# Kernel tuning notes

Measured on AMD Instinct MI355X. Metric: run time of the kernel, lower is better.

The kernel has to match this reference:

```python
import jax, jax.numpy as jnp
import numpy as np

N = 100000
E = 1600000
H = 64      # hidden_size
NH = 8      # num_heads
DH = H // NH  # per-head dim (heads are the LAST axis, as in the torch code)


def _lin(x, W, b):
    return x @ W + b


def setup_inputs() -> dict:
    key = jax.random.key(0)
    ks = jax.random.split(key, 18)
    s = 0.05
    inp = {
        "h_x": jax.random.normal(ks[0], (N, H), jnp.float32),
        "h_e": jax.random.normal(ks[1], (E, H), jnp.float32),
        "row": jax.random.randint(ks[2], (E,), 0, N, jnp.int32),  # dst node of each nonzero
        "col": jax.random.randint(ks[3], (E,), 0, N, jnp.int32),  # src node of each nonzero
    }
    names = ["q", "k", "v", "e", "oh", "oe"]
    for i, nm in enumerate(names):
        inp["W" + nm] = jax.random.normal(ks[4 + 2 * i], (H, H), jnp.float32) * s
        inp["b" + nm] = jax.random.normal(ks[5 + 2 * i], (H,), jnp.float32) * s
    return inp


def reference(h_x, h_e, row, col, Wq, bq, Wk, bk, Wv, bv, We, be, Woh, boh, Woe, boe):
    n = h_x.shape[0]
    m = h_e.shape[0]
    q = _lin(h_x, Wq, bq).reshape(n, DH, NH)
    k = _lin(h_x, Wk, bk).reshape(n, DH, NH)
    v = _lin(h_x, Wv, bv).reshape(n, DH, NH)
    e = _lin(h_e, We, be).reshape(m, DH, NH)

    # SDDMM: per-nonzero (i=row, j=col), per-head dot of q[i] and k[j]  -> (E, NH)
    scores = (q[row] * k[col]).sum(axis=1) / jnp.sqrt(jnp.float32(DH))

    # edge gating: e.sum over dh axis -> (E, NH)
    e_gate = e.sum(axis=1)
    scores = scores * e_gate

    # oe branch (uses pre-softmax gated scores)
    oe_feat = scores[:, None, :] * e          # (E, DH, NH)
    oe = _lin(oe_feat.reshape(m, H), Woe, boe)

    # sparse softmax over dim=1 (per destination row), per head
    mx = jax.ops.segment_max(scores, row, num_segments=n)      # (N, NH)
    ex = jnp.exp(scores - mx[row])
    den = jax.ops.segment_sum(ex, row, num_segments=n)         # (N, NH)
    sm = ex / den[row]                                          # (E, NH)

    # bSpMM: h_out[i,:,h] = sum_{e: row[e]=i} sm[e,h] * v[col[e],:,h]
    h_out = jax.ops.segment_sum(sm[:, None, :] * v[col], row, num_segments=n)
    oh = _lin(h_out.reshape(n, H), Woh, boh)
    return (oh, oe)
```

## Files before the change

kernel.cpp:

```cpp
#include <hip/hip_runtime.h>

typedef __attribute__((ext_vector_type(8))) short bf16x8;
typedef __attribute__((ext_vector_type(4))) float f32x4;
typedef __attribute__((ext_vector_type(4))) unsigned short u16x4;

__device__ __forceinline__ float bf2f(unsigned short h) {
  return __uint_as_float(((unsigned)h) << 16);
}
__device__ __forceinline__ unsigned cvtpk(float a, float b) {
  unsigned r;
  asm("v_cvt_pk_bf16_f32 %0, %1, %2" : "=v"(r) : "v"(a), "v"(b));
  return r;
}
__device__ __forceinline__ unsigned short f2bf(float f) {
  return (unsigned short)(cvtpk(f, f) & 0xffffu);
}
__device__ __forceinline__ bf16x8 pack8(f32x4 x0, f32x4 x1) {
  union { bf16x8 v; unsigned u[4]; } z;
  z.u[0] = cvtpk(x0[0], x0[1]);
  z.u[1] = cvtpk(x0[2], x0[3]);
  z.u[2] = cvtpk(x1[0], x1[1]);
  z.u[3] = cvtpk(x1[2], x1[3]);
  return z.v;
}

template<bool IN_BF16, bool OUT_BF16>
__global__ void __launch_bounds__(256) gemm64_kernel(const void* __restrict__ Ain,
    const float* __restrict__ W, const float* __restrict__ bias,
    void* __restrict__ Out, int M) {
  const int tid = threadIdx.x;
  const int l = tid & 63;
  const int g = l >> 4;
  const int n15 = l & 15;

  bf16x8 bfrag[4][2];
  float bv[4];
#pragma unroll
  for (int nb = 0; nb < 4; ++nb) {
    bv[nb] = bias[nb * 16 + n15];
#pragma unroll
    for (int kb = 0; kb < 2; ++kb)
#pragma unroll
      for (int j = 0; j < 8; ++j)
        bfrag[nb][kb][j] = (short)f2bf(W[(kb * 32 + g * 8 + j) * 64 + nb * 16 + n15]);
  }

  int wid = (blockIdx.x * blockDim.x + tid) >> 6;
  int nw = (gridDim.x * blockDim.x) >> 6;
  int ntiles = (M + 15) >> 4;
  for (int t = wid; t < ntiles; t += nw) {
    int m0 = t << 4;
    int arow = m0 + n15;
    bf16x8 a0, a1;
    if (arow < M) {
      if constexpr (IN_BF16) {
        const unsigned short* ap = (const unsigned short*)Ain + (size_t)arow * 64 + g * 8;
        a0 = *(const bf16x8*)ap;
        a1 = *(const bf16x8*)(ap + 32);
      } else {
        const float* ap = (const float*)Ain + (size_t)arow * 64 + g * 8;
        a0 = pack8(*(const f32x4*)ap, *(const f32x4*)(ap + 4));
        a1 = pack8(*(const f32x4*)(ap + 32), *(const f32x4*)(ap + 36));
      }
    } else {
#pragma unroll
      for (int j = 0; j < 8; ++j) { a0[j] = 0; a1[j] = 0; }
    }
    f32x4 acc[4];
#pragma unroll
    for (int nb = 0; nb < 4; ++nb) {
      acc[nb] = (f32x4){bv[nb], bv[nb], bv[nb], bv[nb]};
      acc[nb] = __builtin_amdgcn_mfma_f32_16x16x32_bf16(a0, bfrag[nb][0], acc[nb], 0, 0, 0);
      acc[nb] = __builtin_amdgcn_mfma_f32_16x16x32_bf16(a1, bfrag[nb][1], acc[nb], 0, 0, 0);
    }
#pragma unroll
    for (int nb = 0; nb < 4; ++nb)
#pragma unroll
      for (int r = 0; r < 4; ++r) {
        int orow = m0 + g * 4 + r;
        if (orow < M) {
          float val = acc[nb][r];
          size_t oidx = (size_t)orow * 64 + nb * 16 + n15;
          if constexpr (OUT_BF16) ((unsigned short*)Out)[oidx] = f2bf(val);
          else                    ((float*)Out)[oidx] = val;
        }
      }
  }
}

__global__ void __launch_bounds__(256) qkv3_kernel(const float* __restrict__ hx,
    const float* __restrict__ Wq, const float* __restrict__ bq,
    const float* __restrict__ Wk, const float* __restrict__ bk,
    const float* __restrict__ Wv, const float* __restrict__ bv,
    unsigned short* __restrict__ q, unsigned short* __restrict__ k,
    unsigned short* __restrict__ v, int M) {
  const int tid = threadIdx.x;
  const int l = tid & 63;
  const int g = l >> 4;
  const int n15 = l & 15;
  const float* Ws[3] = {Wq, Wk, Wv};
  const float* bs[3] = {bq, bk, bv};
  unsigned short* outs[3] = {q, k, v};

  bf16x8 bfrag[3][4][2];
  float bvv[3][4];
#pragma unroll
  for (int w = 0; w < 3; ++w)
#pragma unroll
    for (int nb = 0; nb < 4; ++nb) {
      bvv[w][nb] = bs[w][nb * 16 + n15];
#pragma unroll
      for (int kb = 0; kb < 2; ++kb)
#pragma unroll
        for (int j = 0; j < 8; ++j)
          bfrag[w][nb][kb][j] = (short)f2bf(Ws[w][(kb * 32 + g * 8 + j) * 64 + nb * 16 + n15]);
    }

  int wid = (blockIdx.x * blockDim.x + tid) >> 6;
  int nw = (gridDim.x * blockDim.x) >> 6;
  int ntiles = (M + 15) >> 4;
  for (int t = wid; t < ntiles; t += nw) {
    int m0 = t << 4;
    int arow = m0 + n15;
    bf16x8 a0, a1;
    if (arow < M) {
      const float* ap = hx + (size_t)arow * 64 + g * 8;
      a0 = pack8(*(const f32x4*)ap, *(const f32x4*)(ap + 4));
      a1 = pack8(*(const f32x4*)(ap + 32), *(const f32x4*)(ap + 36));
    } else {
#pragma unroll
      for (int j = 0; j < 8; ++j) { a0[j] = 0; a1[j] = 0; }
    }
#pragma unroll
    for (int w = 0; w < 3; ++w) {
      f32x4 acc[4];
#pragma unroll
      for (int nb = 0; nb < 4; ++nb) {
        acc[nb] = (f32x4){bvv[w][nb], bvv[w][nb], bvv[w][nb], bvv[w][nb]};
        acc[nb] = __builtin_amdgcn_mfma_f32_16x16x32_bf16(a0, bfrag[w][nb][0], acc[nb], 0, 0, 0);
        acc[nb] = __builtin_amdgcn_mfma_f32_16x16x32_bf16(a1, bfrag[w][nb][1], acc[nb], 0, 0, 0);
      }
#pragma unroll
      for (int nb = 0; nb < 4; ++nb)
#pragma unroll
        for (int r = 0; r < 4; ++r) {
          int orow = m0 + g * 4 + r;
          if (orow < M)
            outs[w][(size_t)orow * 64 + nb * 16 + n15] = f2bf(acc[nb][r]);
        }
    }
  }
}

__global__ void __launch_bounds__(512) edge_fused_kernel(
    const float* __restrict__ he,
    const int* __restrict__ rowi, const int* __restrict__ coli,
    const int* __restrict__ eslot,
    const unsigned short* __restrict__ qb, const unsigned short* __restrict__ kbuf,
    const float* __restrict__ We, const float* __restrict__ be,
    const float* __restrict__ Woe, const float* __restrict__ boe,
    float* __restrict__ oe, float* __restrict__ escores, int E) {
  const int tid = threadIdx.x;
  const int wv = tid >> 6;
  const int l = tid & 63;
  const int g = l >> 4;
  const int n15 = l & 15;
  const int h = n15 & 7;

  __shared__ unsigned short WeT[4096];
  __shared__ unsigned short WoT[4096];
  __shared__ float s_lds[8][160];
  __shared__ unsigned short feat_lds[8][16 * 72];

  {
    const int c = tid >> 3, d0 = (tid & 7) * 8;
    const unsigned off = (unsigned)(c * 128 + d0 * 2) ^ ((unsigned)(c & 7) << 4);
    unsigned short* we = (unsigned short*)((char*)WeT + off);
    unsigned short* wo = (unsigned short*)((char*)WoT + off);
#pragma unroll
    for (int j = 0; j < 8; ++j) {
      we[j] = f2bf(We[(d0 + j) * 64 + c]);
      wo[j] = f2bf(Woe[(d0 + j) * 64 + c]);
    }
  }
  float beV[4], boV[4];
#pragma unroll
  for (int nb = 0; nb < 4; ++nb) {
    beV[nb] = be[nb * 16 + n15];
    boV[nb] = boe[nb * 16 + n15];
  }
  __syncthreads();

  const int ntiles = (E + 15) >> 4;
  const int nwav = gridDim.x * 8;
  for (int t = blockIdx.x * 8 + wv; t < ntiles; t += nwav) {
    const int m0 = t << 4;
    const int es = min(m0 + n15, E - 1);
    const int rq = rowi[es], rc = coli[es], sl = eslot[es];

    const float* ap = he + (size_t)es * 64 + g * 8;
    bf16x8 a0 = pack8(*(const f32x4*)ap, *(const f32x4*)(ap + 4));
    bf16x8 a1 = pack8(*(const f32x4*)(ap + 32), *(const f32x4*)(ap + 36));

    const unsigned short* qp = qb + (size_t)rq * 64 + g * 16;
    const unsigned short* kp = kbuf + (size_t)rc * 64 + g * 16;
    bf16x8 qv0 = *(const bf16x8*)qp, qv1 = *(const bf16x8*)(qp + 8);
    bf16x8 kv0 = *(const bf16x8*)kp, kv1 = *(const bf16x8*)(kp + 8);

    f32x4 acc[4];
#pragma unroll
    for (int nb = 0; nb < 4; ++nb) {
      const unsigned off0 = (unsigned)((nb * 16 + n15) * 128 + g * 16)
                            ^ ((unsigned)(n15 & 7) << 4);
      bf16x8 b0 = *(const bf16x8*)((const char*)WeT + off0);
      bf16x8 b1 = *(const bf16x8*)((const char*)WeT + (off0 ^ 64u));
      acc[nb] = (f32x4){beV[nb], beV[nb], beV[nb], beV[nb]};
      acc[nb] = __builtin_amdgcn_mfma_f32_16x16x32_bf16(a0, b0, acc[nb], 0, 0, 0);
      acc[nb] = __builtin_amdgcn_mfma_f32_16x16x32_bf16(a1, b1, acc[nb], 0, 0, 0);
    }
    float gc[4];
#pragma unroll
    for (int r = 0; r < 4; ++r) {
      float s = acc[0][r] + acc[1][r] + acc[2][r] + acc[3][r];
      s += __shfl_xor(s, 8, 64);
      gc[r] = s * 0.35355339059327373f;
    }
    float p[8];
#pragma unroll
    for (int j = 0; j < 8; ++j)
      p[j] = bf2f((unsigned short)qv0[j]) * bf2f((unsigned short)kv0[j])
           + bf2f((unsigned short)qv1[j]) * bf2f((unsigned short)kv1[j]);
#pragma unroll
    for (int j = 0; j < 8; ++j) {
      p[j] += __shfl_xor(p[j], 16, 64);
      p[j] += __shfl_xor(p[j], 32, 64);
    }
    if (l < 16) {
      float2* sp = (float2*)&s_lds[wv][n15 * 10];
#pragma unroll
      for (int j = 0; j < 4; ++j) sp[j] = make_float2(p[2 * j], p[2 * j + 1]);
    }
    float srow[4];
#pragma unroll
    for (int r = 0; r < 4; ++r)
      srow[r] = s_lds[wv][(g * 4 + r) * 10 + h] * gc[r];
#pragma unroll
    for (int r = 0; r < 4; ++r) {
      int slot = __shfl(sl, g * 4 + r, 64);
      if (n15 < 8 && m0 + g * 4 + r < E) escores[(size_t)slot * 8 + n15] = srow[r];
    }
#pragma unroll
    for (int nb = 0; nb < 4; ++nb)
#pragma unroll
      for (int r = 0; r < 4; ++r)
        feat_lds[wv][(g * 4 + r) * 72 + nb * 16 + n15] = f2bf(srow[r] * acc[nb][r]);
    const unsigned short* fpt = &feat_lds[wv][n15 * 72 + g * 8];
    a0 = *(const bf16x8*)fpt;
    a1 = *(const bf16x8*)(fpt + 32);
#pragma unroll
    for (int nb = 0; nb < 4; ++nb) {
      const unsigned off0 = (unsigned)((nb * 16 + n15) * 128 + g * 16)
                            ^ ((unsigned)(n15 & 7) << 4);
      bf16x8 b0 = *(const bf16x8*)((const char*)WoT + off0);
      bf16x8 b1 = *(const bf16x8*)((const char*)WoT + (off0 ^ 64u));
      f32x4 c2 = (f32x4){boV[nb], boV[nb], boV[nb], boV[nb]};
      c2 = __builtin_amdgcn_mfma_f32_16x16x32_bf16(a0, b0, c2, 0, 0, 0);
      c2 = __builtin_amdgcn_mfma_f32_16x16x32_bf16(a1, b1, c2, 0, 0, 0);
#pragma unroll
      for (int r = 0; r < 4; ++r) {
        int orow = m0 + g * 4 + r;
        if (orow < E) oe[(size_t)orow * 64 + nb * 16 + n15] = c2[r];
      }
    }
  }
}

__global__ void zero_kernel(int* __restrict__ p, int n) {
  int i = blockIdx.x * blockDim.x + threadIdx.x;
  if (i < n) p[i] = 0;
}

__global__ void hist_kernel(const int* __restrict__ row, int* __restrict__ deg, int E) {
  int gid = blockIdx.x * blockDim.x + threadIdx.x;
  if (gid < E) atomicAdd(&deg[row[gid]], 1);
}

#define SCAN_B 256
#define SCAN_E 8
__global__ void scan1_kernel(const int* __restrict__ deg, int* __restrict__ rowptr,
                             int* __restrict__ blksum, int n) {
  __shared__ int sh[SCAN_B];
  int base = blockIdx.x * (SCAN_B * SCAN_E) + threadIdx.x * SCAN_E;
  int v[SCAN_E];
  int s = 0;
#pragma unroll
  for (int j = 0; j < SCAN_E; ++j) {
    v[j] = (base + j < n) ? deg[base + j] : 0;
    s += v[j];
  }
  sh[threadIdx.x] = s;
  __syncthreads();
  for (int off = 1; off < SCAN_B; off <<= 1) {
    int t = (threadIdx.x >= off) ? sh[threadIdx.x - off] : 0;
    __syncthreads();
    sh[threadIdx.x] += t;
    __syncthreads();
  }
  if (threadIdx.x == SCAN_B - 1) blksum[blockIdx.x] = sh[SCAN_B - 1];
  int run = sh[threadIdx.x] - s;
#pragma unroll
  for (int j = 0; j < SCAN_E; ++j) {
    if (base + j < n) rowptr[base + j] = run;
    run += v[j];
  }
}

__global__ void scan2_kernel(int* __restrict__ blksum, int nb) {
  __shared__ int sh[SCAN_B];
  int v = (threadIdx.x < nb) ? blksum[threadIdx.x] : 0;
  sh[threadIdx.x] = v;
  __syncthreads();
  for (int off = 1; off < SCAN_B; off <<= 1) {
    int t = (threadIdx.x >= off) ? sh[threadIdx.x - off] : 0;
    __syncthreads();
    sh[threadIdx.x] += t;
    __syncthreads();
  }
  if (threadIdx.x < nb) blksum[threadIdx.x] = sh[threadIdx.x] - v;
}

__global__ void scan3_kernel(int* __restrict__ rowptr, int* __restrict__ cursor,
                             const int* __restrict__ blksum, int n) {
  int i = blockIdx.x * blockDim.x + threadIdx.x;
  if (i >= n) return;
  int v = rowptr[i] + blksum[i / (SCAN_B * SCAN_E)];
  rowptr[i] = v;
  cursor[i] = v;
}

__global__ void scatter_kernel(const int* __restrict__ row, const int* __restrict__ col,
                               int* __restrict__ cursor, int* __restrict__ eslot,
                               int* __restrict__ ecol, int E) {
  int gid = blockIdx.x * blockDim.x + threadIdx.x;
  if (gid >= E) return;
  int r = row[gid];
  int slot = atomicAdd(&cursor[r], 1);
  eslot[gid] = slot;
  ecol[slot] = col[gid];
}

__global__ void __launch_bounds__(256) row_attn_kernel(const float* __restrict__ escores,
    const int* __restrict__ rowptr, const int* __restrict__ deg,
    const int* __restrict__ ecol,
    const unsigned short* __restrict__ vb, float* __restrict__ hout, int n) {
  int gid = blockIdx.x * blockDim.x + threadIdx.x;
  int r = gid >> 6, lane = threadIdx.x & 63;
  if (r >= n) return;
  int gi = lane >> 4, j = lane & 15;
  int start = rowptr[r], dg = deg[r];

  f32x4 acc = (f32x4){0.f, 0.f, 0.f, 0.f};
  f32x4 den = (f32x4){0.f, 0.f, 0.f, 0.f};
  for (int i = gi; i < dg; i += 4) {
    int idx = start + i;
    int c = ecol[idx];
    f32x4 sv = *(const f32x4*)(escores + (size_t)idx * 8 + 4 * (j & 1));
    u16x4 vv = *(const u16x4*)(vb + (size_t)c * 64 + j * 4);
#pragma unroll
    for (int m = 0; m < 4; ++m) {
      float ex = __expf(sv[m]);
      den[m] += ex;
      acc[m] += ex * bf2f(vv[m]);
    }
  }
#pragma unroll
  for (int m = 0; m < 4; ++m) {
    acc[m] += __shfl_xor(acc[m], 16, 64);
    acc[m] += __shfl_xor(acc[m], 32, 64);
    den[m] += __shfl_xor(den[m], 16, 64);
    den[m] += __shfl_xor(den[m], 32, 64);
  }
  if (gi == 0) {
    f32x4 o;
#pragma unroll
    for (int m = 0; m < 4; ++m) o[m] = (dg > 0) ? acc[m] / den[m] : 0.f;
    *(f32x4*)(hout + (size_t)r * 64 + j * 4) = o;
  }
}

extern "C" void kernel_launch(void* const* d_in, const int* in_sizes, int n_in,
                              void* d_out, int out_size, void* d_ws, size_t ws_size,
                              hipStream_t stream) {
  const float* hx  = (const float*)d_in[0];
  const float* he  = (const float*)d_in[1];
  const int*   row = (const int*)d_in[2];
  const int*   col = (const int*)d_in[3];
  const float* Wq = (const float*)d_in[4],  *bq = (const float*)d_in[5];
  const float* Wk = (const float*)d_in[6],  *bk = (const float*)d_in[7];
  const float* Wv = (const float*)d_in[8],  *bv = (const float*)d_in[9];
  const float* We = (const float*)d_in[10], *be = (const float*)d_in[11];
  const float* Woh = (const float*)d_in[12], *boh = (const float*)d_in[13];
  const float* Woe = (const float*)d_in[14], *boe = (const float*)d_in[15];

  const int n = in_sizes[0] / 64;
  const int E = in_sizes[2];

  float* out = (float*)d_out;
  float* oh = out;
  float* oe = out + (size_t)n * 64;

  unsigned short* qb   = (unsigned short*)d_ws;
  unsigned short* kb   = qb + (size_t)n * 64;
  unsigned short* vbuf = kb + (size_t)n * 64;
  float* escores = (float*)(vbuf + (size_t)n * 64);
  float* hout    = escores + (size_t)E * 8;

  int* deg    = (int*)(hout + (size_t)n * 64);
  int* rowptr = deg + n;
  int* cursor = rowptr + n;
  int* blksum = cursor + n;
  int* eslot  = blksum + 256;
  int* ecol   = eslot + (size_t)E;

  const int nb_scan = (n + SCAN_B * SCAN_E - 1) / (SCAN_B * SCAN_E);

  zero_kernel<<<(n + 255) / 256, 256, 0, stream>>>(deg, n);
  hist_kernel<<<(E + 255) / 256, 256, 0, stream>>>(row, deg, E);
  scan1_kernel<<<nb_scan, SCAN_B, 0, stream>>>(deg, rowptr, blksum, n);
  scan2_kernel<<<1, SCAN_B, 0, stream>>>(blksum, nb_scan);
  scan3_kernel<<<(n + 255) / 256, 256, 0, stream>>>(rowptr, cursor, blksum, n);
  scatter_kernel<<<(E + 255) / 256, 256, 0, stream>>>(row, col, cursor, eslot, ecol, E);

  qkv3_kernel<<<512, 256, 0, stream>>>(hx, Wq, bq, Wk, bk, Wv, bv, qb, kb, vbuf, n);
  edge_fused_kernel<<<1024, 512, 0, stream>>>(he, row, col, eslot, qb, kb, We, be,
                                              Woe, boe, oe, escores, E);

  row_attn_kernel<<<(n + 3) / 4, 256, 0, stream>>>(escores, rowptr, deg, ecol,
                                                   vbuf, hout, n);
  gemm64_kernel<false, false><<<512, 256, 0, stream>>>(hout, Woh, boh, oh, n);
}
```

Measured before the change: 555.7 us.

## Split oe GEMM out of edge kernel and co-schedule it with row attention

The Woe projection leaves the fused edge kernel. The edge kernel now writes gated features in bf16 to a workspace buffer, and a combo kernel runs the oe GEMM on some blocks while the remaining blocks do row attention concurrently. Inside the edge kernel, the per-head gate sum is folded into a precomputed reduced weight (WeM/beM) applied via MFMA, and the q·k per-head reduction also uses an MFMA against a selector matrix. This removes the LDS staging and shuffles. The cost is an extra E×64 bf16 write and read, and bf16 rounding of the q·k products before they are summed.

```diff
diff --git a/kernel.cpp b/kernel.cpp
--- a/kernel.cpp
+++ b/kernel.cpp
@@ -25,10 +25,9 @@
 }
 
 template<bool IN_BF16, bool OUT_BF16>
-__global__ void __launch_bounds__(256) gemm64_kernel(const void* __restrict__ Ain,
+__device__ __forceinline__ void gemm64_body(const void* __restrict__ Ain,
     const float* __restrict__ W, const float* __restrict__ bias,
-    void* __restrict__ Out, int M) {
-  const int tid = threadIdx.x;
+    void* __restrict__ Out, int M, int wid, int nw, int tid) {
   const int l = tid & 63;
   const int g = l >> 4;
   const int n15 = l & 15;
@@ -45,8 +44,6 @@
         bfrag[nb][kb][j] = (short)f2bf(W[(kb * 32 + g * 8 + j) * 64 + nb * 16 + n15]);
   }
 
-  int wid = (blockIdx.x * blockDim.x + tid) >> 6;
-  int nw = (gridDim.x * blockDim.x) >> 6;
   int ntiles = (M + 15) >> 4;
   for (int t = wid; t < ntiles; t += nw) {
     int m0 = t << 4;
@@ -88,6 +85,15 @@
   }
 }
 
+template<bool IN_BF16, bool OUT_BF16>
+__global__ void __launch_bounds__(256) gemm64_kernel(const void* __restrict__ Ain,
+    const float* __restrict__ W, const float* __restrict__ bias,
+    void* __restrict__ Out, int M) {
+  int wid = (blockIdx.x * blockDim.x + threadIdx.x) >> 6;
+  int nw = (gridDim.x * blockDim.x) >> 6;
+  gemm64_body<IN_BF16, OUT_BF16>(Ain, W, bias, Out, M, wid, nw, threadIdx.x);
+}
+
 __global__ void __launch_bounds__(256) qkv3_kernel(const float* __restrict__ hx,
     const float* __restrict__ Wq, const float* __restrict__ bq,
     const float* __restrict__ Wk, const float* __restrict__ bk,
@@ -152,48 +158,62 @@
   }
 }
 
-__global__ void __launch_bounds__(512) edge_fused_kernel(
+__global__ void wemprep_kernel(const float* __restrict__ We, const float* __restrict__ be,
+                               float* __restrict__ WeM, float* __restrict__ beM) {
+  int tid = threadIdx.x;
+  if (tid < 512) {
+    int d = tid >> 3, h = tid & 7;
+    float s = 0.f;
+#pragma unroll
+    for (int m = 0; m < 8; ++m) s += We[d * 64 + m * 8 + h];
+    WeM[d * 8 + h] = s * 0.35355339059327373f;
+  }
+  if (tid < 8) {
+    float s = 0.f;
+#pragma unroll
+    for (int m = 0; m < 8; ++m) s += be[tid + m * 8];
+    beM[tid] = s * 0.35355339059327373f;
+  }
+}
+
+__global__ void __launch_bounds__(256) edge_fused_kernel(
     const float* __restrict__ he,
     const int* __restrict__ rowi, const int* __restrict__ coli,
     const int* __restrict__ eslot,
     const unsigned short* __restrict__ qb, const unsigned short* __restrict__ kbuf,
     const float* __restrict__ We, const float* __restrict__ be,
-    const float* __restrict__ Woe, const float* __restrict__ boe,
-    float* __restrict__ oe, float* __restrict__ escores, int E) {
+    const float* __restrict__ WeM, const float* __restrict__ beM,
+    unsigned short* __restrict__ feat, float* __restrict__ escores, int E) {
   const int tid = threadIdx.x;
-  const int wv = tid >> 6;
   const int l = tid & 63;
   const int g = l >> 4;
   const int n15 = l & 15;
-  const int h = n15 & 7;
-
-  __shared__ unsigned short WeT[4096];
-  __shared__ unsigned short WoT[4096];
-  __shared__ float s_lds[8][160];
-  __shared__ unsigned short feat_lds[8][16 * 72];
-
-  {
-    const int c = tid >> 3, d0 = (tid & 7) * 8;
-    const unsigned off = (unsigned)(c * 128 + d0 * 2) ^ ((unsigned)(c & 7) << 4);
-    unsigned short* we = (unsigned short*)((char*)WeT + off);
-    unsigned short* wo = (unsigned short*)((char*)WoT + off);
-#pragma unroll
-    for (int j = 0; j < 8; ++j) {
-      we[j] = f2bf(We[(d0 + j) * 64 + c]);
-      wo[j] = f2bf(Woe[(d0 + j) * 64 + c]);
-    }
-  }
-  float beV[4], boV[4];
+
+  bf16x8 bfE[4][2];
+  float beV[4];
 #pragma unroll
   for (int nb = 0; nb < 4; ++nb) {
     beV[nb] = be[nb * 16 + n15];
-    boV[nb] = boe[nb * 16 + n15];
-  }
-  __syncthreads();
+#pragma unroll
+    for (int kb = 0; kb < 2; ++kb)
+#pragma unroll
+      for (int j = 0; j < 8; ++j)
+        bfE[nb][kb][j] = (short)f2bf(We[(kb * 32 + g * 8 + j) * 64 + nb * 16 + n15]);
+  }
+  bf16x8 gB0, gB1, mB;
+  const bool hv = (n15 < 8);
+#pragma unroll
+  for (int j = 0; j < 8; ++j) {
+    gB0[j] = hv ? (short)f2bf(WeM[(g * 8 + j) * 8 + n15]) : (short)0;
+    gB1[j] = hv ? (short)f2bf(WeM[(32 + g * 8 + j) * 8 + n15]) : (short)0;
+    mB[j]  = (hv && j == n15) ? (short)0x3F80 : (short)0;
+  }
+  const float beMv = hv ? beM[n15] : 0.f;
 
   const int ntiles = (E + 15) >> 4;
-  const int nwav = gridDim.x * 8;
-  for (int t = blockIdx.x * 8 + wv; t < ntiles; t += nwav) {
+  int wid = (blockIdx.x * blockDim.x + tid) >> 6;
+  int nw = (gridDim.x * blockDim.x) >> 6;
+  for (int t = wid; t < ntiles; t += nw) {
     const int m0 = t << 4;
     const int es = min(m0 + n15, E - 1);
     const int rq = rowi[es], rc = coli[es], sl = eslot[es];
@@ -202,76 +222,55 @@
     bf16x8 a0 = pack8(*(const f32x4*)ap, *(const f32x4*)(ap + 4));
     bf16x8 a1 = pack8(*(const f32x4*)(ap + 32), *(const f32x4*)(ap + 36));
 
-    const unsigned short* qp = qb + (size_t)rq * 64 + g * 16;
-    const unsigned short* kp = kbuf + (size_t)rc * 64 + g * 16;
-    bf16x8 qv0 = *(const bf16x8*)qp, qv1 = *(const bf16x8*)(qp + 8);
-    bf16x8 kv0 = *(const bf16x8*)kp, kv1 = *(const bf16x8*)(kp + 8);
+    const unsigned short* qp = qb + (size_t)rq * 64 + g * 8;
+    const unsigned short* kp = kbuf + (size_t)rc * 64 + g * 8;
+    bf16x8 qv0 = *(const bf16x8*)qp, qv1 = *(const bf16x8*)(qp + 32);
+    bf16x8 kv0 = *(const bf16x8*)kp, kv1 = *(const bf16x8*)(kp + 32);
 
     f32x4 acc[4];
 #pragma unroll
     for (int nb = 0; nb < 4; ++nb) {
-      const unsigned off0 = (unsigned)((nb * 16 + n15) * 128 + g * 16)
-                            ^ ((unsigned)(n15 & 7) << 4);
-      bf16x8 b0 = *(const bf16x8*)((const char*)WeT + off0);
-      bf16x8 b1 = *(const bf16x8*)((const char*)WeT + (off0 ^ 64u));
       acc[nb] = (f32x4){beV[nb], beV[nb], beV[nb], beV[nb]};
-      acc[nb] = __builtin_amdgcn_mfma_f32_16x16x32_bf16(a0, b0, acc[nb], 0, 0, 0);
-      acc[nb] = __builtin_amdgcn_mfma_f32_16x16x32_bf16(a1, b1, acc[nb], 0, 0, 0);
-    }
-    float gc[4];
-#pragma unroll
-    for (int r = 0; r < 4; ++r) {
-      float s = acc[0][r] + acc[1][r] + acc[2][r] + acc[3][r];
-      s += __shfl_xor(s, 8, 64);
-      gc[r] = s * 0.35355339059327373f;
-    }
-    float p[8];
-#pragma unroll
-    for (int j = 0; j < 8; ++j)
-      p[j] = bf2f((unsigned short)qv0[j]) * bf2f((unsigned short)kv0[j])
-           + bf2f((unsigned short)qv1[j]) * bf2f((unsigned short)kv1[j]);
-#pragma unroll
-    for (int j = 0; j < 8; ++j) {
-      p[j] += __shfl_xor(p[j], 16, 64);
-      p[j] += __shfl_xor(p[j], 32, 64);
-    }
-    if (l < 16) {
-      float2* sp = (float2*)&s_lds[wv][n15 * 10];
-#pragma unroll
-      for (int j = 0; j < 4; ++j) sp[j] = make_float2(p[2 * j], p[2 * j + 1]);
-    }
-    float srow[4];
-#pragma unroll
-    for (int r = 0; r < 4; ++r)
-      srow[r] = s_lds[wv][(g * 4 + r) * 10 + h] * gc[r];
+      acc[nb] = __builtin_amdgcn_mfma_f32_16x16x32_bf16(a0, bfE[nb][0], acc[nb], 0, 0, 0);
+      acc[nb] = __builtin_amdgcn_mfma_f32_16x16x32_bf16(a1, bfE[nb][1], acc[nb], 0, 0, 0);
+    }
+    f32x4 gate = (f32x4){beMv, beMv, beMv, beMv};
+    gate = __builtin_amdgcn_mfma_f32_16x16x32_bf16(a0, gB0, gate, 0, 0, 0);
+    gate = __builtin_amdgcn_mfma_f32_16x16x32_bf16(a1, gB1, gate, 0, 0, 0);
+
+    f32x4 pr0a, pr0b, pr1a, pr1b;
+#pragma unroll
+    for (int j = 0; j < 4; ++j) {
+      pr0a[j] = bf2f((unsigned short)qv0[j]) * bf2f((unsigned short)kv0[j]);
+      pr0b[j] = bf2f((unsigned short)qv0[4 + j]) * bf2f((unsigned short)kv0[4 + j]);
+      pr1a[j] = bf2f((unsigned short)qv1[j]) * bf2f((unsigned short)kv1[j]);
+      pr1b[j] = bf2f((unsigned short)qv1[4 + j]) * bf2f((unsigned short)kv1[4 + j]);
+    }
+    bf16x8 pa0 = pack8(pr0a, pr0b), pa1 = pack8(pr1a, pr1b);
+    f32x4 p = (f32x4){0.f, 0.f, 0.f, 0.f};
+    p = __builtin_amdgcn_mfma_f32_16x16x32_bf16(pa0, mB, p, 0, 0, 0);
+    p = __builtin_amdgcn_mfma_f32_16x16x32_bf16(pa1, mB, p, 0, 0, 0);
+
+    float s_[4];
+#pragma unroll
+    for (int r = 0; r < 4; ++r) s_[r] = p[r] * gate[r];
 #pragma unroll
     for (int r = 0; r < 4; ++r) {
       int slot = __shfl(sl, g * 4 + r, 64);
-      if (n15 < 8 && m0 + g * 4 + r < E) escores[(size_t)slot * 8 + n15] = srow[r];
+      if (hv && m0 + g * 4 + r < E) escores[(size_t)slot * 8 + n15] = s_[r];
+    }
+#pragma unroll
+    for (int r = 0; r < 4; ++r) {
+      float o = __shfl_xor(s_[r], 8, 64);
+      if (!hv) s_[r] = o;
     }
 #pragma unroll
     for (int nb = 0; nb < 4; ++nb)
-#pragma unroll
-      for (int r = 0; r < 4; ++r)
-        feat_lds[wv][(g * 4 + r) * 72 + nb * 16 + n15] = f2bf(srow[r] * acc[nb][r]);
-    const unsigned short* fpt = &feat_lds[wv][n15 * 72 + g * 8];
-    a0 = *(const bf16x8*)fpt;
-    a1 = *(const bf16x8*)(fpt + 32);
-#pragma unroll
-    for (int nb = 0; nb < 4; ++nb) {
-      const unsigned off0 = (unsigned)((nb * 16 + n15) * 128 + g * 16)
-                            ^ ((unsigned)(n15 & 7) << 4);
-      bf16x8 b0 = *(const bf16x8*)((const char*)WoT + off0);
-      bf16x8 b1 = *(const bf16x8*)((const char*)WoT + (off0 ^ 64u));
-      f32x4 c2 = (f32x4){boV[nb], boV[nb], boV[nb], boV[nb]};
-      c2 = __builtin_amdgcn_mfma_f32_16x16x32_bf16(a0, b0, c2, 0, 0, 0);
-      c2 = __builtin_amdgcn_mfma_f32_16x16x32_bf16(a1, b1, c2, 0, 0, 0);
 #pragma unroll
       for (int r = 0; r < 4; ++r) {
         int orow = m0 + g * 4 + r;
-        if (orow < E) oe[(size_t)orow * 64 + nb * 16 + n15] = c2[r];
+        if (orow < E) feat[(size_t)orow * 64 + nb * 16 + n15] = f2bf(s_[r] * acc[nb][r]);
       }
-    }
   }
 }
 
@@ -349,42 +348,52 @@
   ecol[slot] = col[gid];
 }
 
-__global__ void __launch_bounds__(256) row_attn_kernel(const float* __restrict__ escores,
-    const int* __restrict__ rowptr, const int* __restrict__ deg,
-    const int* __restrict__ ecol,
+__global__ void __launch_bounds__(256) combo_kernel(
+    const unsigned short* __restrict__ feat, const float* __restrict__ Woe,
+    const float* __restrict__ boe, float* __restrict__ oe, int E,
+    const float* __restrict__ escores, const int* __restrict__ rowptr,
+    const int* __restrict__ deg, const int* __restrict__ ecol,
     const unsigned short* __restrict__ vb, float* __restrict__ hout, int n) {
-  int gid = blockIdx.x * blockDim.x + threadIdx.x;
-  int r = gid >> 6, lane = threadIdx.x & 63;
-  if (r >= n) return;
+  const int nOe = (gridDim.x * 3) >> 3;
+  if ((int)blockIdx.x < nOe) {
+    int wid = (blockIdx.x * blockDim.x + threadIdx.x) >> 6;
+    int nw = (nOe * blockDim.x) >> 6;
+    gemm64_body<true, false>(feat, Woe, boe, oe, E, wid, nw, threadIdx.x);
+    return;
+  }
+  const int nAttn = gridDim.x - nOe;
+  int bid = blockIdx.x - nOe;
+  int lane = threadIdx.x & 63;
   int gi = lane >> 4, j = lane & 15;
-  int start = rowptr[r], dg = deg[r];
-
-  f32x4 acc = (f32x4){0.f, 0.f, 0.f, 0.f};
-  f32x4 den = (f32x4){0.f, 0.f, 0.f, 0.f};
-  for (int i = gi; i < dg; i += 4) {
-    int idx = start + i;
-    int c = ecol[idx];
-    f32x4 sv = *(const f32x4*)(escores + (size_t)idx * 8 + 4 * (j & 1));
-    u16x4 vv = *(const u16x4*)(vb + (size_t)c * 64 + j * 4);
+  for (int r = bid * 4 + (threadIdx.x >> 6); r < n; r += nAttn * 4) {
+    int start = rowptr[r], dg = deg[r];
+    f32x4 acc = (f32x4){0.f, 0.f, 0.f, 0.f};
+    f32x4 den = (f32x4){0.f, 0.f, 0.f, 0.f};
+    for (int i = gi; i < dg; i += 4) {
+      int idx = start + i;
+      int c = ecol[idx];
+      f32x4 sv = *(const f32x4*)(escores + (size_t)idx * 8 + 4 * (j & 1));
+      u16x4 vv = *(const u16x4*)(vb + (size_t)c * 64 + j * 4);
+#pragma unroll
+      for (int m = 0; m < 4; ++m) {
+        float ex = __expf(sv[m]);
+        den[m] += ex;
+        acc[m] += ex * bf2f(vv[m]);
+      }
+    }
 #pragma unroll
     for (int m = 0; m < 4; ++m) {
-      float ex = __expf(sv[m]);
-      den[m] += ex;
-      acc[m] += ex * bf2f(vv[m]);
-    }
-  }
-#pragma unroll
-  for (int m = 0; m < 4; ++m) {
-    acc[m] += __shfl_xor(acc[m], 16, 64);
-    acc[m] += __shfl_xor(acc[m], 32, 64);
-    den[m] += __shfl_xor(den[m], 16, 64);
-    den[m] += __shfl_xor(den[m], 32, 64);
-  }
-  if (gi == 0) {
-    f32x4 o;
-#pragma unroll
-    for (int m = 0; m < 4; ++m) o[m] = (dg > 0) ? acc[m] / den[m] : 0.f;
-    *(f32x4*)(hout + (size_t)r * 64 + j * 4) = o;
+      acc[m] += __shfl_xor(acc[m], 16, 64);
+      acc[m] += __shfl_xor(acc[m], 32, 64);
+      den[m] += __shfl_xor(den[m], 16, 64);
+      den[m] += __shfl_xor(den[m], 32, 64);
+    }
+    if (gi == 0) {
+      f32x4 o;
+#pragma unroll
+      for (int m = 0; m < 4; ++m) o[m] = (dg > 0) ? acc[m] / den[m] : 0.f;
+      *(f32x4*)(hout + (size_t)r * 64 + j * 4) = o;
+    }
   }
 }
 
@@ -421,6 +430,9 @@
   int* blksum = cursor + n;
   int* eslot  = blksum + 256;
   int* ecol   = eslot + (size_t)E;
+  unsigned short* feat = (unsigned short*)(ecol + (size_t)E);
+  float* WeM = (float*)(feat + (size_t)E * 64);
+  float* beM = WeM + 512;
 
   const int nb_scan = (n + SCAN_B * SCAN_E - 1) / (SCAN_B * SCAN_E);
 
@@ -432,10 +444,13 @@
   scatter_kernel<<<(E + 255) / 256, 256, 0, stream>>>(row, col, cursor, eslot, ecol, E);
 
   qkv3_kernel<<<512, 256, 0, stream>>>(hx, Wq, bq, Wk, bk, Wv, bv, qb, kb, vbuf, n);
-  edge_fused_kernel<<<1024, 512, 0, stream>>>(he, row, col, eslot, qb, kb, We, be,
-                                              Woe, boe, oe, escores, E);
-
-  row_attn_kernel<<<(n + 3) / 4, 256, 0, stream>>>(escores, rowptr, deg, ecol,
-                                                   vbuf, hout, n);
+  wemprep_kernel<<<1, 512, 0, stream>>>(We, be, WeM, beM);
+
+  edge_fused_kernel<<<2048, 256, 0, stream>>>(he, row, col, eslot, qb, kb, We, be,
+                                              WeM, beM, feat, escores, E);
+
+  combo_kernel<<<4096, 256, 0, stream>>>(feat, Woe, boe, oe, E,
+                                         escores, rowptr, deg, ecol, vbuf, hout, n);
+
   gemm64_kernel<false, false><<<512, 256, 0, stream>>>(hout, Woh, boh, oh, n);
 }
```

After: 745.7 us. 1.34x slower.
